# Optimization experiments

Measured on AMD Instinct MI355X. Metric: run time of the kernel, lower is better.

Reference implementation:

```python
import jax, jax.numpy as jnp
import numpy as np


def _squash(s, eps=1e-8):
    # s: [b, j, n]; standard capsule squash: ||s||^2/(1+||s||^2) * s/||s||
    sq = jnp.sum(s * s, axis=-1, keepdims=True)
    return s * (sq / (1.0 + sq)) / jnp.sqrt(sq + eps)


def setup_inputs() -> dict:
    key = jax.random.key(0)
    k1, = jax.random.split(key, 1)
    b, j, i, n = 64, 32, 4096, 16
    u_hat = jax.random.normal(k1, (b, j, i, n), dtype=jnp.float32)
    bias = jnp.full((j, n), 0.1, dtype=jnp.float32)  # nn.Parameter filled with 0.1
    return {"u_hat": u_hat, "bias": bias, "iters": 3}


def reference(u_hat, bias, iters):
    b, j, i, n = u_hat.shape
    b_vec = jnp.zeros((b, j, i), dtype=u_hat.dtype)
    entropies = []
    v_vec = None
    for idx in range(iters):
        # routing coefficients: softmax over parent capsules (dim=1)
        c_vec = jax.nn.softmax(b_vec, axis=1)  # [b, j, i]
        # entropy over parent dim, averaged over child caps -> [b]
        ent = -jnp.sum(c_vec * jnp.log(c_vec), axis=1).mean(axis=1)
        entropies.append(ent)
        # weighted sum of predictions: [b, j, n]
        s_vec = jnp.einsum('bji,bjin->bjn', c_vec, u_hat)
        s_vec_bias = s_vec + bias  # broadcast [j, n]
        reset_mask = jnp.sum(s_vec, axis=2) == 0  # [b, j]
        s_vec_bias = jnp.where(reset_mask[..., None], 0.0, s_vec_bias)
        v_vec = _squash(s_vec_bias)  # [b, j, n]
        if idx < iters - 1:
            # agreement update: dot(u_hat, v_vec) over n -> [b, j, i]
            b_vec = b_vec + jnp.einsum('bjin,bjn->bji', u_hat, v_vec)
    entropy_layer = jnp.stack(entropies, axis=1)  # [b, iters]
    return v_vec, entropy_layer
```

## Files before the change

### kernel.cpp

```cpp
#include <hip/hip_runtime.h>
#include <hip/hip_fp16.h>
#include <math.h>


#define WS_S0   0
#define WS_S1   32768
#define WS_S2   65536
#define WS_V0   98304
#define WS_W    131072
#define WS_ENT  163840
#define WS_TOTAL 164032
#define WS_U16  262144

union H2U { unsigned u; __half2 h; };

__global__ __launch_bounds__(256) void k_colsum(const float* __restrict__ u,
                                                __half* __restrict__ u16,
                                                float* __restrict__ s0) {
  const int bj = blockIdx.x;
  const int t  = threadIdx.x;
  const float4* base = (const float4*)u + (size_t)bj * 16384;
  uint2* out = (uint2*)u16 + (size_t)bj * 16384;
  float4 acc = make_float4(0.f, 0.f, 0.f, 0.f);
  #pragma unroll 4
  for (int k = 0; k < 64; ++k) {
    const int idx = t + k * 256;
    const float4 x = base[idx];
    acc.x += x.x; acc.y += x.y; acc.z += x.z; acc.w += x.w;
    H2U p0, p1;
    p0.h = __float22half2_rn(make_float2(x.x, x.y));
    p1.h = __float22half2_rn(make_float2(x.z, x.w));
    out[idx] = make_uint2(p0.u, p1.u);
  }
  __shared__ float4 red4[256];
  red4[t] = acc;
  __syncthreads();
  if (t < 16) {
    const float* red = (const float*)red4;
    float s = 0.f;
    #pragma unroll
    for (int r = 0; r < 64; ++r) s += red[r * 16 + t];
    s0[bj * 16 + t] = s;
  }
}

__device__ __forceinline__ void squash16(float* sb, const float* __restrict__ bias,
                                         int j, float* out16) {
  float ssum = 0.f;
  #pragma unroll
  for (int n = 0; n < 16; ++n) ssum += sb[n];
  if (ssum == 0.f) {
    #pragma unroll
    for (int n = 0; n < 16; ++n) out16[n] = 0.f;
    return;
  }
  float sq = 0.f;
  #pragma unroll
  for (int n = 0; n < 16; ++n) { sb[n] += bias[j * 16 + n]; sq += sb[n] * sb[n]; }
  const float f = sq / ((1.f + sq) * sqrtf(sq + 1e-8f));
  #pragma unroll
  for (int n = 0; n < 16; ++n) out16[n] = sb[n] * f;
}

__global__ __launch_bounds__(256) void k_v0(const float* __restrict__ s0,
                                            const float* __restrict__ bias,
                                            float* __restrict__ v0) {
  const int bj = blockIdx.x * 256 + threadIdx.x;
  const int j = bj & 31;
  float sb[16], out[16];
  #pragma unroll
  for (int n = 0; n < 16; ++n) sb[n] = s0[bj * 16 + n] * (1.f / 32.f);
  squash16(sb, bias, j, out);
  #pragma unroll
  for (int n = 0; n < 16; ++n) v0[bj * 16 + n] = out[n];
}

__global__ __launch_bounds__(256) void k_v1(const float* __restrict__ s1,
                                            const float* __restrict__ bias,
                                            const float* __restrict__ v0,
                                            float* __restrict__ wv) {
  const int bj = blockIdx.x * 256 + threadIdx.x;
  const int j = bj & 31;
  float sb[16], out[16];
  #pragma unroll
  for (int n = 0; n < 16; ++n) sb[n] = s1[bj * 16 + n];
  squash16(sb, bias, j, out);
  #pragma unroll
  for (int n = 0; n < 16; ++n) wv[bj * 16 + n] = v0[bj * 16 + n] + out[n];
}

__global__ __launch_bounds__(256) void k_final(const float* __restrict__ s2,
                                               const float* __restrict__ bias,
                                               const float* __restrict__ ent,
                                               float* __restrict__ out) {
  const int bj = blockIdx.x * 256 + threadIdx.x;
  const int j = bj & 31;
  float sb[16], v[16];
  #pragma unroll
  for (int n = 0; n < 16; ++n) sb[n] = s2[bj * 16 + n];
  squash16(sb, bias, j, v);
  float4* o4 = (float4*)(out + bj * 16);
  o4[0] = make_float4(v[0], v[1], v[2], v[3]);
  o4[1] = make_float4(v[4], v[5], v[6], v[7]);
  o4[2] = make_float4(v[8], v[9], v[10], v[11]);
  o4[3] = make_float4(v[12], v[13], v[14], v[15]);
  if (bj < 64) {
    out[32768 + bj * 3 + 0] = logf(32.f);
    out[32768 + bj * 3 + 1] = ent[bj * 3 + 1] * (1.f / 4096.f);
    out[32768 + bj * 3 + 2] = ent[bj * 3 + 2] * (1.f / 4096.f);
  }
}

__global__ __launch_bounds__(256) void k_route(const __half* __restrict__ u16,
                                               const float* __restrict__ vv,
                                               float* __restrict__ s_out,
                                               float* __restrict__ ent_ws,
                                               int iter) {
  const int b  = blockIdx.y;
  const int i0 = blockIdx.x * 256;
  const int t  = threadIdx.x;
  const int w  = t >> 6;
  const int ln = t & 63;
  const int jl = t & 31;
  const int grp = t >> 5;

  __shared__ __align__(16) unsigned char u_raw[32 * 1040];
  __shared__ float v_l[512];

  if (t < 128) ((float4*)v_l)[t] = ((const float4*)vv)[b * 128 + t];
  __syncthreads();
  float vr[16];
  #pragma unroll
  for (int n = 0; n < 16; ++n) vr[n] = v_l[jl * 16 + n];

  const uint4* gbase = (const uint4*)u16 + (size_t)(b * 32) * 8192;
  uint4 r[8];
  #pragma unroll
  for (int L = 0; L < 8; ++L)
    r[L] = gbase[(size_t)(L * 4 + w) * 8192 + (size_t)i0 * 2 + ln];

  float acc[16];
  #pragma unroll
  for (int n = 0; n < 16; ++n) acc[n] = 0.f;
  float ent_acc = 0.f;

  for (int tt = 0; tt < 8; ++tt) {
    __syncthreads();
    #pragma unroll
    for (int L = 0; L < 8; ++L)
      *(uint4*)(u_raw + (L * 4 + w) * 1040 + ln * 16) = r[L];
    __syncthreads();

    if (tt < 7) {
      #pragma unroll
      for (int L = 0; L < 8; ++L)
        r[L] = gbase[(size_t)(L * 4 + w) * 8192 + (size_t)(i0 + (tt + 1) * 32) * 2 + ln];
    }

    #pragma unroll
    for (int q = 0; q < 4; ++q) {
      const int il = grp * 4 + q;
      const unsigned char* row = u_raw + jl * 1040 + il * 32;
      const uint4 da = *(const uint4*)(row);
      const uint4 db = *(const uint4*)(row + 16);
      float f[16];
      {
        H2U h; float2 p;
        h.u = da.x; p = __half22float2(h.h); f[0] = p.x;  f[1] = p.y;
        h.u = da.y; p = __half22float2(h.h); f[2] = p.x;  f[3] = p.y;
        h.u = da.z; p = __half22float2(h.h); f[4] = p.x;  f[5] = p.y;
        h.u = da.w; p = __half22float2(h.h); f[6] = p.x;  f[7] = p.y;
        h.u = db.x; p = __half22float2(h.h); f[8] = p.x;  f[9] = p.y;
        h.u = db.y; p = __half22float2(h.h); f[10] = p.x; f[11] = p.y;
        h.u = db.z; p = __half22float2(h.h); f[12] = p.x; f[13] = p.y;
        h.u = db.w; p = __half22float2(h.h); f[14] = p.x; f[15] = p.y;
      }
      float a = 0.f;
      #pragma unroll
      for (int n = 0; n < 16; ++n) a += f[n] * vr[n];

      float m = a;
      #pragma unroll
      for (int msk = 16; msk >= 1; msk >>= 1) m = fmaxf(m, __shfl_xor(m, msk, 32));
      const float e = expf(a - m);
      float Z = e, S = e * (a - m);
      #pragma unroll
      for (int msk = 16; msk >= 1; msk >>= 1) {
        Z += __shfl_xor(Z, msk, 32);
        S += __shfl_xor(S, msk, 32);
      }
      const float rZ = 1.f / Z;
      const float c = e * rZ;
      ent_acc += logf(Z) - S * rZ;
      #pragma unroll
      for (int n = 0; n < 16; ++n) acc[n] += c * f[n];
    }
  }

  __syncthreads();
  float* red = (float*)u_raw;
  #pragma unroll
  for (int n = 0; n < 16; ++n) red[(grp * 32 + jl) * 17 + n] = acc[n];
  __syncthreads();
  const int jo = t >> 3, np = t & 7;
  float s0v = 0.f, s1v = 0.f;
  #pragma unroll
  for (int g = 0; g < 8; ++g) {
    s0v += red[(g * 32 + jo) * 17 + np * 2];
    s1v += red[(g * 32 + jo) * 17 + np * 2 + 1];
  }
  atomicAdd(&s_out[(b * 32 + jo) * 16 + np * 2],     s0v);
  atomicAdd(&s_out[(b * 32 + jo) * 16 + np * 2 + 1], s1v);

  float e = ent_acc;
  e += __shfl_xor(e, 32);
  if (ln == 0) atomicAdd(&ent_ws[b * 3 + iter], e);
}

extern "C" void kernel_launch(void* const* d_in, const int* in_sizes, int n_in,
                              void* d_out, int out_size, void* d_ws, size_t ws_size,
                              hipStream_t stream) {
  const float* u    = (const float*)d_in[0];
  const float* bias = (const float*)d_in[1];
  float* out = (float*)d_out;
  float* ws  = (float*)d_ws;
  __half* u16 = (__half*)(ws + WS_U16);

  hipMemsetAsync(d_ws, 0, WS_TOTAL * sizeof(float), stream);

  k_colsum<<<2048, 256, 0, stream>>>(u, u16, ws + WS_S0);
  k_v0<<<8, 256, 0, stream>>>(ws + WS_S0, bias, ws + WS_V0);
  k_route<<<dim3(16, 64), 256, 0, stream>>>(u16, ws + WS_V0, ws + WS_S1, ws + WS_ENT, 1);
  k_v1<<<8, 256, 0, stream>>>(ws + WS_S1, bias, ws + WS_V0, ws + WS_W);
  k_route<<<dim3(16, 64), 256, 0, stream>>>(u16, ws + WS_W, ws + WS_S2, ws + WS_ENT, 2);
  k_final<<<8, 256, 0, stream>>>(ws + WS_S2, bias, ws + WS_ENT, out);
}
```

Before: 963.2 us.

## Fuse squash kernels into routing kernel and use nontemporal loads

Removes the separate k_v0 and k_v1 launches. Each routing block now recomputes the squashed v vectors for its batch from the raw s sums, and issues its global u16 loads before that computation so they overlap it. Nontemporal loads are used for the fp32 input read in colsum and for the last routing pass, which keeps that single-use data from displacing cached lines. The memset is narrowed to the accumulators that need zeroing. The cost is redundant squash work in every block (16 blocks per batch).

```diff
diff --git a/kernel.cpp b/kernel.cpp
--- a/kernel.cpp
+++ b/kernel.cpp
@@ -6,11 +6,12 @@
 #define WS_S0   0
 #define WS_S1   32768
 #define WS_S2   65536
-#define WS_V0   98304
-#define WS_W    131072
-#define WS_ENT  163840
-#define WS_TOTAL 164032
+#define WS_ENT  98304
+#define WS_ZERO_FLOATS (65536 + 192)
 #define WS_U16  262144
+
+typedef float  f4v __attribute__((ext_vector_type(4)));
+typedef unsigned u4v __attribute__((ext_vector_type(4)));
 
 union H2U { unsigned u; __half2 h; };
 
@@ -19,20 +20,20 @@
                                                 float* __restrict__ s0) {
   const int bj = blockIdx.x;
   const int t  = threadIdx.x;
-  const float4* base = (const float4*)u + (size_t)bj * 16384;
+  const f4v* base = (const f4v*)u + (size_t)bj * 16384;
   uint2* out = (uint2*)u16 + (size_t)bj * 16384;
-  float4 acc = make_float4(0.f, 0.f, 0.f, 0.f);
+  f4v acc = {0.f, 0.f, 0.f, 0.f};
   #pragma unroll 4
   for (int k = 0; k < 64; ++k) {
     const int idx = t + k * 256;
-    const float4 x = base[idx];
-    acc.x += x.x; acc.y += x.y; acc.z += x.z; acc.w += x.w;
+    const f4v x = __builtin_nontemporal_load(base + idx);
+    acc += x;
     H2U p0, p1;
     p0.h = __float22half2_rn(make_float2(x.x, x.y));
     p1.h = __float22half2_rn(make_float2(x.z, x.w));
     out[idx] = make_uint2(p0.u, p1.u);
   }
-  __shared__ float4 red4[256];
+  __shared__ f4v red4[256];
   red4[t] = acc;
   __syncthreads();
   if (t < 16) {
@@ -62,60 +63,13 @@
   for (int n = 0; n < 16; ++n) out16[n] = sb[n] * f;
 }
 
-__global__ __launch_bounds__(256) void k_v0(const float* __restrict__ s0,
-                                            const float* __restrict__ bias,
-                                            float* __restrict__ v0) {
-  const int bj = blockIdx.x * 256 + threadIdx.x;
-  const int j = bj & 31;
-  float sb[16], out[16];
-  #pragma unroll
-  for (int n = 0; n < 16; ++n) sb[n] = s0[bj * 16 + n] * (1.f / 32.f);
-  squash16(sb, bias, j, out);
-  #pragma unroll
-  for (int n = 0; n < 16; ++n) v0[bj * 16 + n] = out[n];
-}
-
-__global__ __launch_bounds__(256) void k_v1(const float* __restrict__ s1,
-                                            const float* __restrict__ bias,
-                                            const float* __restrict__ v0,
-                                            float* __restrict__ wv) {
-  const int bj = blockIdx.x * 256 + threadIdx.x;
-  const int j = bj & 31;
-  float sb[16], out[16];
-  #pragma unroll
-  for (int n = 0; n < 16; ++n) sb[n] = s1[bj * 16 + n];
-  squash16(sb, bias, j, out);
-  #pragma unroll
-  for (int n = 0; n < 16; ++n) wv[bj * 16 + n] = v0[bj * 16 + n] + out[n];
-}
-
-__global__ __launch_bounds__(256) void k_final(const float* __restrict__ s2,
+__global__ __launch_bounds__(256) void k_route(const __half* __restrict__ u16,
+                                               const float* __restrict__ s0,
+                                               const float* __restrict__ s1,
                                                const float* __restrict__ bias,
-                                               const float* __restrict__ ent,
-                                               float* __restrict__ out) {
-  const int bj = blockIdx.x * 256 + threadIdx.x;
-  const int j = bj & 31;
-  float sb[16], v[16];
-  #pragma unroll
-  for (int n = 0; n < 16; ++n) sb[n] = s2[bj * 16 + n];
-  squash16(sb, bias, j, v);
-  float4* o4 = (float4*)(out + bj * 16);
-  o4[0] = make_float4(v[0], v[1], v[2], v[3]);
-  o4[1] = make_float4(v[4], v[5], v[6], v[7]);
-  o4[2] = make_float4(v[8], v[9], v[10], v[11]);
-  o4[3] = make_float4(v[12], v[13], v[14], v[15]);
-  if (bj < 64) {
-    out[32768 + bj * 3 + 0] = logf(32.f);
-    out[32768 + bj * 3 + 1] = ent[bj * 3 + 1] * (1.f / 4096.f);
-    out[32768 + bj * 3 + 2] = ent[bj * 3 + 2] * (1.f / 4096.f);
-  }
-}
-
-__global__ __launch_bounds__(256) void k_route(const __half* __restrict__ u16,
-                                               const float* __restrict__ vv,
                                                float* __restrict__ s_out,
                                                float* __restrict__ ent_ws,
-                                               int iter) {
+                                               int iter, int last) {
   const int b  = blockIdx.y;
   const int i0 = blockIdx.x * 256;
   const int t  = threadIdx.x;
@@ -127,17 +81,34 @@
   __shared__ __align__(16) unsigned char u_raw[32 * 1040];
   __shared__ float v_l[512];
 
-  if (t < 128) ((float4*)v_l)[t] = ((const float4*)vv)[b * 128 + t];
+  const u4v* gbase = (const u4v*)u16 + (size_t)(b * 32) * 8192;
+  u4v r[8];
+  #pragma unroll
+  for (int L = 0; L < 8; ++L)
+    r[L] = last ? __builtin_nontemporal_load(gbase + (size_t)(L * 4 + w) * 8192 + (size_t)i0 * 2 + ln)
+                : gbase[(size_t)(L * 4 + w) * 8192 + (size_t)i0 * 2 + ln];
+
+  if (t < 32) {
+    const int j = t;
+    float sb[16], vout[16];
+    #pragma unroll
+    for (int n = 0; n < 16; ++n) sb[n] = s0[b * 512 + j * 16 + n] * (1.f / 32.f);
+    squash16(sb, bias, j, vout);
+    if (s1 != nullptr) {
+      float sb1[16], v1[16];
+      #pragma unroll
+      for (int n = 0; n < 16; ++n) sb1[n] = s1[b * 512 + j * 16 + n];
+      squash16(sb1, bias, j, v1);
+      #pragma unroll
+      for (int n = 0; n < 16; ++n) vout[n] += v1[n];
+    }
+    #pragma unroll
+    for (int n = 0; n < 16; ++n) v_l[j * 16 + n] = vout[n];
+  }
   __syncthreads();
   float vr[16];
   #pragma unroll
   for (int n = 0; n < 16; ++n) vr[n] = v_l[jl * 16 + n];
-
-  const uint4* gbase = (const uint4*)u16 + (size_t)(b * 32) * 8192;
-  uint4 r[8];
-  #pragma unroll
-  for (int L = 0; L < 8; ++L)
-    r[L] = gbase[(size_t)(L * 4 + w) * 8192 + (size_t)i0 * 2 + ln];
 
   float acc[16];
   #pragma unroll
@@ -148,21 +119,23 @@
     __syncthreads();
     #pragma unroll
     for (int L = 0; L < 8; ++L)
-      *(uint4*)(u_raw + (L * 4 + w) * 1040 + ln * 16) = r[L];
+      *(u4v*)(u_raw + (L * 4 + w) * 1040 + ln * 16) = r[L];
     __syncthreads();
 
     if (tt < 7) {
       #pragma unroll
-      for (int L = 0; L < 8; ++L)
-        r[L] = gbase[(size_t)(L * 4 + w) * 8192 + (size_t)(i0 + (tt + 1) * 32) * 2 + ln];
+      for (int L = 0; L < 8; ++L) {
+        const size_t gi = (size_t)(L * 4 + w) * 8192 + (size_t)(i0 + (tt + 1) * 32) * 2 + ln;
+        r[L] = last ? __builtin_nontemporal_load(gbase + gi) : gbase[gi];
+      }
     }
 
     #pragma unroll
     for (int q = 0; q < 4; ++q) {
       const int il = grp * 4 + q;
       const unsigned char* row = u_raw + jl * 1040 + il * 32;
-      const uint4 da = *(const uint4*)(row);
-      const uint4 db = *(const uint4*)(row + 16);
+      const u4v da = *(const u4v*)(row);
+      const u4v db = *(const u4v*)(row + 16);
       float f[16];
       {
         H2U h; float2 p;
@@ -217,6 +190,28 @@
   if (ln == 0) atomicAdd(&ent_ws[b * 3 + iter], e);
 }
 
+__global__ __launch_bounds__(256) void k_final(const float* __restrict__ s2,
+                                               const float* __restrict__ bias,
+                                               const float* __restrict__ ent,
+                                               float* __restrict__ out) {
+  const int bj = blockIdx.x * 256 + threadIdx.x;
+  const int j = bj & 31;
+  float sb[16], v[16];
+  #pragma unroll
+  for (int n = 0; n < 16; ++n) sb[n] = s2[bj * 16 + n];
+  squash16(sb, bias, j, v);
+  float4* o4 = (float4*)(out + bj * 16);
+  o4[0] = make_float4(v[0], v[1], v[2], v[3]);
+  o4[1] = make_float4(v[4], v[5], v[6], v[7]);
+  o4[2] = make_float4(v[8], v[9], v[10], v[11]);
+  o4[3] = make_float4(v[12], v[13], v[14], v[15]);
+  if (bj < 64) {
+    out[32768 + bj * 3 + 0] = logf(32.f);
+    out[32768 + bj * 3 + 1] = ent[bj * 3 + 1] * (1.f / 4096.f);
+    out[32768 + bj * 3 + 2] = ent[bj * 3 + 2] * (1.f / 4096.f);
+  }
+}
+
 extern "C" void kernel_launch(void* const* d_in, const int* in_sizes, int n_in,
                               void* d_out, int out_size, void* d_ws, size_t ws_size,
                               hipStream_t stream) {
@@ -226,12 +221,12 @@
   float* ws  = (float*)d_ws;
   __half* u16 = (__half*)(ws + WS_U16);
 
-  hipMemsetAsync(d_ws, 0, WS_TOTAL * sizeof(float), stream);
+  hipMemsetAsync(ws + WS_S1, 0, WS_ZERO_FLOATS * sizeof(float), stream);
 
   k_colsum<<<2048, 256, 0, stream>>>(u, u16, ws + WS_S0);
-  k_v0<<<8, 256, 0, stream>>>(ws + WS_S0, bias, ws + WS_V0);
-  k_route<<<dim3(16, 64), 256, 0, stream>>>(u16, ws + WS_V0, ws + WS_S1, ws + WS_ENT, 1);
-  k_v1<<<8, 256, 0, stream>>>(ws + WS_S1, bias, ws + WS_V0, ws + WS_W);
-  k_route<<<dim3(16, 64), 256, 0, stream>>>(u16, ws + WS_W, ws + WS_S2, ws + WS_ENT, 2);
+  k_route<<<dim3(16, 64), 256, 0, stream>>>(u16, ws + WS_S0, nullptr, bias,
+                                            ws + WS_S1, ws + WS_ENT, 1, 0);
+  k_route<<<dim3(16, 64), 256, 0, stream>>>(u16, ws + WS_S0, ws + WS_S1, bias,
+                                            ws + WS_S2, ws + WS_ENT, 2, 1);
   k_final<<<8, 256, 0, stream>>>(ws + WS_S2, bias, ws + WS_ENT, out);
 }
```

Result: faster. 803.2 us (-16.6%).
